# Optimization experiments

Hardware: AMD Instinct MI355X
Metric: run time of the kernel (lower is better)

The kernel has to match this reference:

```python
import jax, jax.numpy as jnp
import numpy as np

B, C1, C2, H, W = 16, 64, 64, 160, 160
K, KS, HID = 4, 3, 16  # K kernels, 3x3, hidden = max(int(64/16),16)=16
EPS = 1e-5


def setup_inputs() -> dict:
    key = jax.random.key(0)
    ks = jax.random.split(key, 8)
    fan_out = KS * KS * C2
    return {
        "x": jax.random.normal(ks[0], (B, C1, H, W), jnp.float32),
        # K candidate conv kernels and biases
        "Wk": jax.random.normal(ks[1], (K, C2, C1, KS, KS), jnp.float32) * np.sqrt(2.0 / fan_out),
        "bk": jnp.zeros((K, C2), jnp.float32),
        # attention trunk: 1x1 conv C1->HID (no bias), BN, ReLU
        "Wfc": jax.random.normal(ks[2], (HID, C1), jnp.float32) * 0.1,
        "gamma_h": jnp.ones((HID,), jnp.float32),
        "beta_h": jnp.zeros((HID,), jnp.float32),
        # four attention heads
        "Wf": jax.random.normal(ks[3], (C2, HID), jnp.float32) * 0.1,
        "bf": jnp.zeros((C2,), jnp.float32),
        "Ws": jax.random.normal(ks[4], (KS * KS, HID), jnp.float32) * 0.1,
        "bs": jnp.zeros((KS * KS,), jnp.float32),
        "Wc": jax.random.normal(ks[5], (C1, HID), jnp.float32) * 0.1,
        "bc": jnp.zeros((C1,), jnp.float32),
        "Ww": jax.random.normal(ks[6], (K, HID), jnp.float32) * 0.1,
        "bw": jnp.zeros((K,), jnp.float32),
        # outer BatchNorm2d params
        "gamma_o": jnp.ones((C2,), jnp.float32),
        "beta_o": jnp.zeros((C2,), jnp.float32),
    }


def reference(x, Wk, bk, Wfc, gamma_h, beta_h, Wf, bf, Ws, bs, Wc, bc, Ww, bw, gamma_o, beta_o):
    # ---- per-sample attention over K kernels ----
    ctx = x.mean(axis=(2, 3))                      # (B, C1)  global avg pool
    h = ctx @ Wfc.T                                # (B, HID) 1x1 conv == linear
    mu = h.mean(axis=0)
    var = h.var(axis=0)                            # biased, as torch BN training
    h = (h - mu) / jnp.sqrt(var + EPS) * gamma_h + beta_h
    h = jax.nn.relu(h)
    attn_f = jax.nn.sigmoid(h @ Wf.T + bf)         # (B, C2)
    attn_s = jax.nn.sigmoid(h @ Ws.T + bs).reshape(B, KS, KS)
    attn_c = jax.nn.sigmoid(h @ Wc.T + bc)         # (B, C1)
    attn_w = jax.nn.softmax(h @ Ww.T + bw, axis=-1)  # (B, K)

    # attn: (B, K, C2, C1, KS, KS) via broadcasting
    attn = (attn_w[:, :, None, None, None, None]
            * attn_f[:, None, :, None, None, None]
            * attn_c[:, None, None, :, None, None]
            * attn_s[:, None, None, None, :, :])
    weight = jnp.sum(attn * Wk[None], axis=1)      # (B, C2, C1, KS, KS)
    bias = attn_w @ bk                             # (B, C2)

    # ---- batched conv as grouped conv with groups=B ----
    out = jax.lax.conv_general_dilated(
        x.reshape(1, B * C1, H, W),
        weight.reshape(B * C2, C1, KS, KS),
        window_strides=(1, 1), padding=((1, 1), (1, 1)),
        dimension_numbers=('NCHW', 'OIHW', 'NCHW'),
        feature_group_count=B)                     # (1, B*C2, H, W)
    out = out.reshape(B, C2, H, W) + bias[:, :, None, None]

    # ---- outer BatchNorm2d (training stats) + SiLU ----
    mu_o = out.mean(axis=(0, 2, 3))
    var_o = out.var(axis=(0, 2, 3))
    out = (out - mu_o[None, :, None, None]) / jnp.sqrt(var_o + EPS)[None, :, None, None]
    out = out * gamma_o[None, :, None, None] + beta_o[None, :, None, None]
    return out * jax.nn.sigmoid(out)               # SiLU
```

## Files before the change

### kernel.cpp

```cpp
#include <hip/hip_runtime.h>
#include <math.h>

#define BB 16
#define C1 64
#define C2 64
#define HH 160
#define WW 160
#define KK 4
#define HID 16
#define EPS 1e-5f
#define HWSZ (HH*WW)
#define NPB (BB*HWSZ)

#define WS_AF    1024
#define WS_AC    2048
#define WS_AS    3072
#define WS_AW    3216
#define WS_BIAS  3280
#define WS_SC    4304
#define WS_SH    4368
#define WS_STATS 4432
#define NSLOT    32
#define WS_PART  8704
#define WS_WEFF  49664
#define WS_XBF   344576

typedef __attribute__((ext_vector_type(8)))  short bf16x8;
typedef __attribute__((ext_vector_type(16))) float f32x16;

__device__ __forceinline__ unsigned short f2bf(float f) {
    unsigned int u = __float_as_uint(f);
    unsigned int r = (u + 0x7FFFu + ((u >> 16) & 1u)) >> 16;
    return (unsigned short)r;
}

__device__ __forceinline__ void gload16(const void* g, void* l) {
    __builtin_amdgcn_global_load_lds(
        (const __attribute__((address_space(1))) unsigned int*)g,
        (__attribute__((address_space(3))) unsigned int*)l, 16, 0, 0);
}

__global__ __launch_bounds__(256) void xprep_kernel(const float* __restrict__ x,
                                                    float* __restrict__ ws) {
    __shared__ float lds[10240];
    int bcc = blockIdx.y;
    int rg = blockIdx.x;
    int t = threadIdx.x;

    const float* src = x + (size_t)bcc * 16 * HWSZ + (size_t)rg * 4 * WW;
    float4* l4 = (float4*)lds;
    #pragma unroll
    for (int i = 0; i < 10; ++i) {
        int g = i * 256 + t;
        int ch = g / 160, rem = g - ch * 160;
        l4[g] = *(const float4*)(src + (size_t)ch * HWSZ + rem * 4);
    }
    __syncthreads();

    {
        int ch = t >> 4, j = t & 15;
        float s = 0.f;
        #pragma unroll
        for (int m = 0; m < 40; ++m) s += lds[ch * 640 + j + 16 * m];
        #pragma unroll
        for (int o = 8; o > 0; o >>= 1) s += __shfl_down(s, o, 16);
        if (j == 0) ws[WS_PART + ((size_t)bcc * 40 + rg) * 16 + ch] = s;
    }

    uint4* dst = (uint4*)(ws + WS_XBF) + ((size_t)bcc * 160 + rg * 4) * 320;
    #pragma unroll
    for (int i = 0; i < 5; ++i) {
        int u = i * 256 + t;
        int row = u / 320, rem = u - row * 320;
        int col = rem >> 1, p = rem & 1;
        int h = p ^ ((col >> 2) & 1) ^ 1;
        union { uint4 q; unsigned short us[8]; } pk;
        #pragma unroll
        for (int k = 0; k < 8; ++k)
            pk.us[k] = f2bf(lds[(h * 8 + k) * 640 + row * 160 + col]);
        dst[u] = pk.q;
    }
}

__global__ void attn_kernel(float* __restrict__ ws,
    const float* __restrict__ Wfc, const float* __restrict__ gh, const float* __restrict__ bh,
    const float* __restrict__ Wf,  const float* __restrict__ bf,
    const float* __restrict__ Wsm, const float* __restrict__ bs,
    const float* __restrict__ Wc,  const float* __restrict__ bc,
    const float* __restrict__ Ww,  const float* __restrict__ bw,
    const float* __restrict__ bk) {
    __shared__ float ctxs[16][64];
    __shared__ float hs[16][16];
    __shared__ float aw[16][4];
    int t = threadIdx.x;

    #pragma unroll
    for (int q = 0; q < 4; ++q) {
        int idx = t * 4 + q;
        int b = idx >> 6, c1 = idx & 63;
        const float* pp = ws + WS_PART + ((size_t)(b * 4 + (c1 >> 4)) * 40) * 16 + (c1 & 15);
        float s = 0.f;
        #pragma unroll
        for (int rg = 0; rg < 40; ++rg) s += pp[rg * 16];
        ctxs[b][c1] = s * (1.0f / (float)HWSZ);
    }
    __syncthreads();
    {
        int b = t >> 4, j = t & 15;
        const float* wr = Wfc + j * 64;
        float s = 0.f;
        #pragma unroll
        for (int c = 0; c < 64; c++) s += ctxs[b][c] * wr[c];
        hs[b][j] = s;
    }
    __syncthreads();
    if (t < 16) {
        int j = t;
        float mu = 0.f;
        #pragma unroll
        for (int b = 0; b < 16; b++) mu += hs[b][j];
        mu *= (1.f / 16.f);
        float vr = 0.f;
        #pragma unroll
        for (int b = 0; b < 16; b++) { float d = hs[b][j] - mu; vr += d * d; }
        vr *= (1.f / 16.f);
        float sc = gh[j] * rsqrtf(vr + EPS);
        float sh = bh[j] - mu * sc;
        #pragma unroll
        for (int b = 0; b < 16; b++) {
            float v = hs[b][j] * sc + sh;
            hs[b][j] = v > 0.f ? v : 0.f;
        }
    }
    __syncthreads();
    if (t < 16) {
        int b = t;
        float l[4]; float mx = -1e30f;
        #pragma unroll
        for (int k = 0; k < 4; k++) {
            float s = bw[k];
            #pragma unroll
            for (int j = 0; j < 16; j++) s += hs[b][j] * Ww[k * 16 + j];
            l[k] = s; mx = fmaxf(mx, s);
        }
        float den = 0.f;
        #pragma unroll
        for (int k = 0; k < 4; k++) { l[k] = expf(l[k] - mx); den += l[k]; }
        float r = 1.f / den;
        #pragma unroll
        for (int k = 0; k < 4; k++) { float v = l[k] * r; aw[b][k] = v; ws[WS_AW + b * 4 + k] = v; }
    }
    #pragma unroll
    for (int q = 0; q < 4; q++) {
        int idx = t * 4 + q;
        int b = idx >> 6, c2 = idx & 63;
        float sf = bf[c2], sc2 = bc[c2];
        #pragma unroll
        for (int j = 0; j < 16; j++) {
            float hv = hs[b][j];
            sf  += hv * Wf[c2 * 16 + j];
            sc2 += hv * Wc[c2 * 16 + j];
        }
        ws[WS_AF + idx] = 1.f / (1.f + expf(-sf));
        ws[WS_AC + idx] = 1.f / (1.f + expf(-sc2));
    }
    if (t < 144) {
        int b = t / 9, uv = t % 9;
        float s = bs[uv];
        #pragma unroll
        for (int j = 0; j < 16; j++) s += hs[b][j] * Wsm[uv * 16 + j];
        ws[WS_AS + t] = 1.f / (1.f + expf(-s));
    }
    __syncthreads();
    #pragma unroll
    for (int q = 0; q < 4; q++) {
        int idx = t * 4 + q;
        int b = idx >> 6, c2 = idx & 63;
        float s = 0.f;
        #pragma unroll
        for (int k = 0; k < 4; k++) s += aw[b][k] * bk[k * 64 + c2];
        ws[WS_BIAS + idx] = s;
    }
    for (int i = t; i < NSLOT * 128; i += 256) ws[WS_STATS + i] = 0.f;
}

__global__ void wprep_kernel(const float* __restrict__ Wk, float* __restrict__ ws) {
    int b = blockIdx.y;
    int tid = blockIdx.x * 256 + threadIdx.x;
    int h = tid & 1;
    int c2 = (tid >> 1) & 63;
    int g = tid >> 7;
    int uv = g % 9;
    int chunk = g / 9;
    const float* awp = ws + WS_AW + b * 4;
    float aw0 = awp[0], aw1 = awp[1], aw2 = awp[2], aw3 = awp[3];
    float af = ws[WS_AF + b * 64 + c2];
    float as_ = ws[WS_AS + b * 9 + uv];
    union { uint4 q; unsigned short u[8]; } pk;
    #pragma unroll
    for (int j = 0; j < 8; ++j) {
        int c1 = chunk * 16 + h * 8 + j;
        const float* wp = Wk + (size_t)(c2 * 64 + c1) * 9 + uv;
        float s = aw0 * wp[0] + aw1 * wp[64 * 64 * 9] + aw2 * wp[2 * 64 * 64 * 9] + aw3 * wp[3 * 64 * 64 * 9];
        float w = s * af * ws[WS_AC + b * 64 + c1] * as_;
        pk.u[j] = f2bf(w);
    }
    int unit = ((chunk * 9 + uv) * 64 + c2) * 2 + (h ^ ((c2 >> 2) & 1));
    ((uint4*)(ws + WS_WEFF))[(size_t)b * 4608 + unit] = pk.q;
}

__launch_bounds__(512, 2)
__global__ void conv_kernel(const float* __restrict__ wsf, float* __restrict__ out) {
    __shared__ uint4 xs[2][6 * 162 * 2];
    __shared__ uint4 wsh[4 * 1152];
    __shared__ float sst[128];

    int id = blockIdx.x;
    int b = id & 15;
    int bx = id >> 4;
    int y0 = bx * 4;
    int t = threadIdx.x;
    int wv = t >> 6;
    int lane = t & 63;
    int l31 = lane & 31;
    int l5 = lane >> 5;
    int c2blk = wv & 1;
    int rw = wv >> 1;

    if (t < 128) sst[t] = 0.f;
    if (t >= 128 && t < 176) {
        int q = t - 128; int bq = q / 24; q %= 24;
        int r = q / 4, side = (q >> 1) & 1, p = q & 1;
        xs[bq][(r * 162 + side * 161) * 2 + p] = make_uint4(0, 0, 0, 0);
    }
    int rbad = (bx == 0) ? 0 : (bx == 39 ? 5 : -1);
    if (rbad >= 0) {
        for (int i = t; i < 640; i += 512)
            xs[i / 320][(rbad * 162 + 1) * 2 + (i % 320)] = make_uint4(0, 0, 0, 0);
    }

    int cb = c2blk * 32 + 4 * l5;
    float bv[16];
    #pragma unroll
    for (int r = 0; r < 16; ++r)
        bv[r] = wsf[WS_BIAS + b * 64 + cb + (r & 3) + 8 * (r >> 2)];

    const uint4* weff = (const uint4*)(wsf + WS_WEFF) + (size_t)b * 4608;
    const uint4* xbf  = (const uint4*)(wsf + WS_XBF);

    auto stage_x = [&](int cc, int bq) {
        for (int i = wv; i < 30; i += 8) {
            int r = i / 5, seg = i % 5;
            int gy = y0 - 1 + r;
            if (gy >= 0 && gy < HH)
                gload16(xbf + (((size_t)b * 4 + cc) * 160 + gy) * 320 + seg * 64 + lane,
                        (char*)&xs[bq][0] + ((r * 162 + 1) * 2 + seg * 64) * 16);
        }
    };

    for (int i = wv; i < 72; i += 8)
        gload16(weff + i * 64 + lane, (char*)wsh + i * 1024);
    stage_x(0, 0);

    f32x16 acc[5];
    #pragma unroll
    for (int j = 0; j < 5; ++j)
        #pragma unroll
        for (int r = 0; r < 16; ++r) acc[j][r] = 0.f;

    __syncthreads();

    int cur = 0;
    int c2 = c2blk * 32 + l31;
    int aswz = (c2 >> 2) & 1;
    for (int cc = 0; cc < 4; ++cc) {
        if (cc < 3) stage_x(cc + 1, cur ^ 1);
        #pragma unroll
        for (int uv = 0; uv < 9; ++uv) {
            bf16x8 a = *(bf16x8*)&wsh[(cc * 576 + uv * 64 + c2) * 2 + (l5 ^ aswz)];
            int xrow = rw + uv / 3;
            int v = uv % 3;
            #pragma unroll
            for (int j = 0; j < 5; ++j) {
                int col = j * 32 + l31 + v;
                bf16x8 bb = *(bf16x8*)&xs[cur][(xrow * 162 + col) * 2 + (l5 ^ (((col + 3) >> 2) & 1))];
                acc[j] = __builtin_amdgcn_mfma_f32_32x32x16_bf16(a, bb, acc[j], 0, 0, 0);
            }
        }
        asm volatile("s_waitcnt vmcnt(0)" ::: "memory");
        __builtin_amdgcn_s_barrier();
        __builtin_amdgcn_sched_barrier(0);
        cur ^= 1;
    }

    float* outb = out + (size_t)b * C2 * HWSZ + (size_t)(y0 + rw) * WW;
    float sr[16], qr[16];
    #pragma unroll
    for (int r = 0; r < 16; ++r) { sr[r] = 0.f; qr[r] = 0.f; }
    #pragma unroll
    for (int j = 0; j < 5; ++j) {
        #pragma unroll
        for (int r = 0; r < 16; ++r) {
            int c2r = cb + (r & 3) + 8 * (r >> 2);
            float v = acc[j][r] + bv[r];
            outb[(size_t)c2r * HWSZ + j * 32 + l31] = v;
            sr[r] += v;
            qr[r] = fmaf(v, v, qr[r]);
        }
    }
    #pragma unroll
    for (int r = 0; r < 16; ++r) {
        float sv = sr[r], qv = qr[r];
        #pragma unroll
        for (int m = 1; m <= 16; m <<= 1) {
            sv += __shfl_xor(sv, m, 64);
            qv += __shfl_xor(qv, m, 64);
        }
        if (l31 == 0) {
            int c2r = cb + (r & 3) + 8 * (r >> 2);
            atomicAdd(&sst[c2r], sv);
            atomicAdd(&sst[64 + c2r], qv);
        }
    }
    __syncthreads();
    if (t < 128) {
        int slot = (b * 40 + bx) & (NSLOT - 1);
        atomicAdd((float*)wsf + WS_STATS + slot * 128 + t, sst[t]);
    }
}

__global__ void bnstat_kernel(float* __restrict__ ws, const float* __restrict__ go,
                              const float* __restrict__ bo) {
    int c = threadIdx.x;
    float s = 0.f, q = 0.f;
    for (int sl = 0; sl < NSLOT; sl++) {
        s += ws[WS_STATS + sl * 128 + c];
        q += ws[WS_STATS + sl * 128 + 64 + c];
    }
    float mu  = s * (1.0f / (float)NPB);
    float var = q * (1.0f / (float)NPB) - mu * mu;
    float sc  = go[c] * rsqrtf(var + EPS);
    ws[WS_SC + c] = sc;
    ws[WS_SH + c] = bo[c] - mu * sc;
}

__global__ void bnact_kernel(float* __restrict__ out, const float* __restrict__ ws) {
    __shared__ float sc[64], sh[64];
    if (threadIdx.x < 64) {
        sc[threadIdx.x] = ws[WS_SC + threadIdx.x];
        sh[threadIdx.x] = ws[WS_SH + threadIdx.x];
    }
    __syncthreads();
    const int n4 = BB * C2 * HWSZ / 4;
    for (int i = blockIdx.x * blockDim.x + threadIdx.x; i < n4; i += gridDim.x * blockDim.x) {
        float4 v = ((float4*)out)[i];
        int c = ((i * 4) / HWSZ) & 63;
        float s = sc[c], h = sh[c];
        v.x = v.x * s + h; v.y = v.y * s + h; v.z = v.z * s + h; v.w = v.w * s + h;
        v.x = v.x / (1.f + __expf(-v.x));
        v.y = v.y / (1.f + __expf(-v.y));
        v.z = v.z / (1.f + __expf(-v.z));
        v.w = v.w / (1.f + __expf(-v.w));
        ((float4*)out)[i] = v;
    }
}

extern "C" void kernel_launch(void* const* d_in, const int* in_sizes, int n_in,
                              void* d_out, int out_size, void* d_ws, size_t ws_size,
                              hipStream_t stream) {
    const float* x   = (const float*)d_in[0];
    const float* Wk  = (const float*)d_in[1];
    const float* bk  = (const float*)d_in[2];
    const float* Wfc = (const float*)d_in[3];
    const float* gh  = (const float*)d_in[4];
    const float* bh  = (const float*)d_in[5];
    const float* Wf  = (const float*)d_in[6];
    const float* bf  = (const float*)d_in[7];
    const float* Wsm = (const float*)d_in[8];
    const float* bs  = (const float*)d_in[9];
    const float* Wc  = (const float*)d_in[10];
    const float* bc  = (const float*)d_in[11];
    const float* Ww  = (const float*)d_in[12];
    const float* bw  = (const float*)d_in[13];
    const float* go  = (const float*)d_in[14];
    const float* bo  = (const float*)d_in[15];
    float* out = (float*)d_out;
    float* ws  = (float*)d_ws;

    xprep_kernel<<<dim3(40, 64), dim3(256), 0, stream>>>(x, ws);
    attn_kernel<<<dim3(1), dim3(256), 0, stream>>>(ws, Wfc, gh, bh, Wf, bf, Wsm, bs, Wc, bc, Ww, bw, bk);
    wprep_kernel<<<dim3(18, 16), dim3(256), 0, stream>>>(Wk, ws);
    conv_kernel<<<dim3(640), dim3(512), 0, stream>>>(ws, out);
    bnstat_kernel<<<dim3(1), dim3(64), 0, stream>>>(ws, go, bo);
    bnact_kernel<<<dim3(2048), dim3(256), 0, stream>>>(out, ws);
}
```

Measured before the change: 146.0 us.

## Halve conv block threads, give each wave both C2 halves, double-buffer weights

Restructures the conv kernel to use 256 threads, with each wave computing all 64 output channels (two MFMA accumulator sets) for one row. This doubles reuse of each loaded x fragment across two weight fragments. Weights are now streamed per channel chunk into a double buffer, while x is single-buffered and staged between two barriers. The epilogue uses a transpose-style shuffle reduction for BN stats, and bias moves to shared memory. The trade-off is more accumulator registers per thread and x loads that are no longer overlapped with compute.

```diff
diff --git a/kernel.cpp b/kernel.cpp
--- a/kernel.cpp
+++ b/kernel.cpp
@@ -209,10 +209,11 @@
     ((uint4*)(ws + WS_WEFF))[(size_t)b * 4608 + unit] = pk.q;
 }
 
-__launch_bounds__(512, 2)
+__launch_bounds__(256, 2)
 __global__ void conv_kernel(const float* __restrict__ wsf, float* __restrict__ out) {
-    __shared__ uint4 xs[2][6 * 162 * 2];
-    __shared__ uint4 wsh[4 * 1152];
+    __shared__ uint4 xs[6 * 162 * 2];
+    __shared__ uint4 wsh[2][1152];
+    __shared__ float bsh[64];
     __shared__ float sst[128];
 
     int id = blockIdx.x;
@@ -224,107 +225,119 @@
     int lane = t & 63;
     int l31 = lane & 31;
     int l5 = lane >> 5;
-    int c2blk = wv & 1;
-    int rw = wv >> 1;
-
-    if (t < 128) sst[t] = 0.f;
-    if (t >= 128 && t < 176) {
-        int q = t - 128; int bq = q / 24; q %= 24;
-        int r = q / 4, side = (q >> 1) & 1, p = q & 1;
-        xs[bq][(r * 162 + side * 161) * 2 + p] = make_uint4(0, 0, 0, 0);
+
+    if (t < 64) bsh[t] = wsf[WS_BIAS + b * 64 + t];
+    if (t >= 64 && t < 128) sst[t - 64] = 0.f;
+    if (t >= 128 && t < 192) sst[t - 64] = 0.f;
+    if (t >= 192 && t < 216) {
+        int q = t - 192;
+        int r = q >> 2, side = (q >> 1) & 1, p = q & 1;
+        xs[(r * 162 + side * 161) * 2 + p] = make_uint4(0, 0, 0, 0);
     }
     int rbad = (bx == 0) ? 0 : (bx == 39 ? 5 : -1);
     if (rbad >= 0) {
-        for (int i = t; i < 640; i += 512)
-            xs[i / 320][(rbad * 162 + 1) * 2 + (i % 320)] = make_uint4(0, 0, 0, 0);
-    }
-
-    int cb = c2blk * 32 + 4 * l5;
-    float bv[16];
-    #pragma unroll
-    for (int r = 0; r < 16; ++r)
-        bv[r] = wsf[WS_BIAS + b * 64 + cb + (r & 3) + 8 * (r >> 2)];
+        for (int i = t; i < 320; i += 256)
+            xs[(rbad * 162 + 1) * 2 + i] = make_uint4(0, 0, 0, 0);
+    }
 
     const uint4* weff = (const uint4*)(wsf + WS_WEFF) + (size_t)b * 4608;
     const uint4* xbf  = (const uint4*)(wsf + WS_XBF);
 
-    auto stage_x = [&](int cc, int bq) {
-        for (int i = wv; i < 30; i += 8) {
+    auto stage_w = [&](int cc, int bq) {
+        for (int i = wv; i < 18; i += 4)
+            gload16(weff + (size_t)cc * 1152 + i * 64 + lane, (char*)&wsh[bq][0] + i * 1024);
+    };
+    auto stage_x = [&](int cc) {
+        for (int i = wv; i < 30; i += 4) {
             int r = i / 5, seg = i % 5;
             int gy = y0 - 1 + r;
             if (gy >= 0 && gy < HH)
                 gload16(xbf + (((size_t)b * 4 + cc) * 160 + gy) * 320 + seg * 64 + lane,
-                        (char*)&xs[bq][0] + ((r * 162 + 1) * 2 + seg * 64) * 16);
+                        (char*)xs + ((r * 162 + 1) * 2 + seg * 64) * 16);
         }
     };
 
-    for (int i = wv; i < 72; i += 8)
-        gload16(weff + i * 64 + lane, (char*)wsh + i * 1024);
-    stage_x(0, 0);
-
-    f32x16 acc[5];
-    #pragma unroll
-    for (int j = 0; j < 5; ++j)
-        #pragma unroll
-        for (int r = 0; r < 16; ++r) acc[j][r] = 0.f;
-
+    f32x16 acc[2][5];
+    #pragma unroll
+    for (int a = 0; a < 2; ++a)
+        #pragma unroll
+        for (int j = 0; j < 5; ++j)
+            #pragma unroll
+            for (int r = 0; r < 16; ++r) acc[a][j][r] = 0.f;
+
+    stage_w(0, 0);
+    stage_x(0);
     __syncthreads();
 
     int cur = 0;
-    int c2 = c2blk * 32 + l31;
-    int aswz = (c2 >> 2) & 1;
+    int aswz = (l31 >> 2) & 1;
     for (int cc = 0; cc < 4; ++cc) {
-        if (cc < 3) stage_x(cc + 1, cur ^ 1);
+        if (cc < 3) stage_w(cc + 1, cur ^ 1);
         #pragma unroll
         for (int uv = 0; uv < 9; ++uv) {
-            bf16x8 a = *(bf16x8*)&wsh[(cc * 576 + uv * 64 + c2) * 2 + (l5 ^ aswz)];
-            int xrow = rw + uv / 3;
+            bf16x8 a0 = *(bf16x8*)&wsh[cur][(uv * 64 + l31) * 2 + (l5 ^ aswz)];
+            bf16x8 a1 = *(bf16x8*)&wsh[cur][(uv * 64 + 32 + l31) * 2 + (l5 ^ aswz)];
+            int xrow = wv + uv / 3;
             int v = uv % 3;
             #pragma unroll
             for (int j = 0; j < 5; ++j) {
                 int col = j * 32 + l31 + v;
-                bf16x8 bb = *(bf16x8*)&xs[cur][(xrow * 162 + col) * 2 + (l5 ^ (((col + 3) >> 2) & 1))];
-                acc[j] = __builtin_amdgcn_mfma_f32_32x32x16_bf16(a, bb, acc[j], 0, 0, 0);
+                bf16x8 bb = *(bf16x8*)&xs[(xrow * 162 + col) * 2 + (l5 ^ (((col + 3) >> 2) & 1))];
+                acc[0][j] = __builtin_amdgcn_mfma_f32_32x32x16_bf16(a0, bb, acc[0][j], 0, 0, 0);
+                acc[1][j] = __builtin_amdgcn_mfma_f32_32x32x16_bf16(a1, bb, acc[1][j], 0, 0, 0);
             }
         }
-        asm volatile("s_waitcnt vmcnt(0)" ::: "memory");
-        __builtin_amdgcn_s_barrier();
-        __builtin_amdgcn_sched_barrier(0);
+        __syncthreads();
+        if (cc < 3) stage_x(cc + 1);
+        __syncthreads();
         cur ^= 1;
     }
 
-    float* outb = out + (size_t)b * C2 * HWSZ + (size_t)(y0 + rw) * WW;
-    float sr[16], qr[16];
-    #pragma unroll
-    for (int r = 0; r < 16; ++r) { sr[r] = 0.f; qr[r] = 0.f; }
-    #pragma unroll
-    for (int j = 0; j < 5; ++j) {
+    float* outb = out + (size_t)b * C2 * HWSZ + (size_t)(y0 + wv) * WW;
+    #pragma unroll
+    for (int a = 0; a < 2; ++a) {
+        float sr[16], qr[16];
         #pragma unroll
         for (int r = 0; r < 16; ++r) {
-            int c2r = cb + (r & 3) + 8 * (r >> 2);
-            float v = acc[j][r] + bv[r];
-            outb[(size_t)c2r * HWSZ + j * 32 + l31] = v;
-            sr[r] += v;
-            qr[r] = fmaf(v, v, qr[r]);
-        }
-    }
-    #pragma unroll
-    for (int r = 0; r < 16; ++r) {
-        float sv = sr[r], qv = qr[r];
-        #pragma unroll
-        for (int m = 1; m <= 16; m <<= 1) {
-            sv += __shfl_xor(sv, m, 64);
-            qv += __shfl_xor(qv, m, 64);
-        }
-        if (l31 == 0) {
-            int c2r = cb + (r & 3) + 8 * (r >> 2);
-            atomicAdd(&sst[c2r], sv);
-            atomicAdd(&sst[64 + c2r], qv);
+            int c2r = a * 32 + (r & 3) + 8 * (r >> 2) + 4 * l5;
+            float bias = bsh[c2r];
+            float s = 0.f, q = 0.f;
+            #pragma unroll
+            for (int j = 0; j < 5; ++j) {
+                float v = acc[a][j][r] + bias;
+                outb[(size_t)c2r * HWSZ + j * 32 + l31] = v;
+                s += v;
+                q = fmaf(v, v, q);
+            }
+            sr[r] = s; qr[r] = q;
+        }
+        #pragma unroll
+        for (int k = 0; k < 4; ++k) {
+            int m = 1 << k, n = 8 >> k;
+            #pragma unroll
+            for (int i = 0; i < 8; ++i) {
+                if (i < n) {
+                    float ks = (l31 & m) ? sr[i + n] : sr[i];
+                    float ss = (l31 & m) ? sr[i] : sr[i + n];
+                    sr[i] = ks + __shfl_xor(ss, m, 64);
+                    float kq = (l31 & m) ? qr[i + n] : qr[i];
+                    float sq = (l31 & m) ? qr[i] : qr[i + n];
+                    qr[i] = kq + __shfl_xor(sq, m, 64);
+                }
+            }
+        }
+        sr[0] += __shfl_xor(sr[0], 16, 64);
+        qr[0] += __shfl_xor(qr[0], 16, 64);
+        if (l31 < 16) {
+            int rf = ((l31 & 1) << 3) | ((l31 & 2) << 1) | ((l31 & 4) >> 1) | ((l31 & 8) >> 3);
+            int c2r = a * 32 + (rf & 3) + 8 * (rf >> 2) + 4 * l5;
+            atomicAdd(&sst[c2r], sr[0]);
+            atomicAdd(&sst[64 + c2r], qr[0]);
         }
     }
     __syncthreads();
     if (t < 128) {
-        int slot = (b * 40 + bx) & (NSLOT - 1);
+        int slot = id & (NSLOT - 1);
         atomicAdd((float*)wsf + WS_STATS + slot * 128 + t, sst[t]);
     }
 }
@@ -390,7 +403,7 @@
     xprep_kernel<<<dim3(40, 64), dim3(256), 0, stream>>>(x, ws);
     attn_kernel<<<dim3(1), dim3(256), 0, stream>>>(ws, Wfc, gh, bh, Wf, bf, Wsm, bs, Wc, bc, Ww, bw, bk);
     wprep_kernel<<<dim3(18, 16), dim3(256), 0, stream>>>(Wk, ws);
-    conv_kernel<<<dim3(640), dim3(512), 0, stream>>>(ws, out);
+    conv_kernel<<<dim3(640), dim3(256), 0, stream>>>(ws, out);
     bnstat_kernel<<<dim3(1), dim3(64), 0, stream>>>(ws, go, bo);
     bnact_kernel<<<dim3(2048), dim3(256), 0, stream>>>(out, ws);
 }
```

Result: faster. 132.4 us (-9.3%).
